# Kernel tuning notes

Hardware: AMD Instinct MI355X
Metric: run time of the kernel (lower is better)

## Reference

```python
import jax, jax.numpy as jnp
import numpy as np

B, S, H = 8, 4096, 1024
E, K = 64, 2
CAP_FACTOR = 1.25
TEMP = 1.0
LBW = 0.01


def setup_inputs() -> dict:
    key = jax.random.key(0)
    k1, k2, k3 = jax.random.split(key, 3)
    x = jax.random.normal(k1, (B, S, H), dtype=jnp.float32)
    gate_w = jax.random.normal(k2, (E, H), dtype=jnp.float32) * 0.02
    expert_w = jax.random.normal(k3, (E, H, H), dtype=jnp.float32) * 0.02
    return {"x": x, "gate_w": gate_w, "expert_w": expert_w}


def _moe_forward(x, gate_w, expert_w):
    b, s, h = x.shape
    xf = x.reshape(-1, h)                      # [N, H]
    N = xf.shape[0]
    capacity = int(N * K / E * CAP_FACTOR)

    # --- gating ---
    logits = xf @ gate_w.T                     # [N, E]
    vals, idx = jax.lax.top_k(logits / TEMP, K)  # [N, K]
    probs = jax.nn.softmax(vals, axis=-1)      # [N, K]

    # --- dispatch: first-come-first-served position within each expert ---
    ef = idx.reshape(-1)                       # [N*K], token-major order (matches torch loop)
    onehot = jax.nn.one_hot(ef, E, dtype=jnp.int32)            # [N*K, E]
    pos = jnp.take_along_axis(jnp.cumsum(onehot, axis=0), ef[:, None], axis=1)[:, 0] - 1
    valid = pos < capacity
    slot = jnp.where(valid, ef * capacity + pos, E * capacity)  # out-of-range -> dropped

    # token_map[e, c] = token_idx * K + k  (or -1 if empty)
    token_map = jnp.full((E * capacity,), -1, dtype=jnp.int32)
    token_map = token_map.at[slot].set(jnp.arange(N * K, dtype=jnp.int32), mode="drop")

    tok = jnp.clip(token_map // K, 0, N - 1)
    filled = token_map >= 0
    expert_inputs = jnp.where(filled[:, None], xf[tok], 0.0)    # [E*cap, H]
    expert_inputs = expert_inputs.reshape(E, capacity, h)

    # --- grouped expert GEMM (no bias; zero rows stay zero) ---
    expert_outputs = jnp.einsum("ech,edh->ecd", expert_inputs, expert_w)  # [E, cap, H]

    # --- combine: weighted scatter-add back to tokens ---
    eo_flat = expert_outputs.reshape(E * capacity, h)
    wk = token_map % K
    weight = jnp.where(filled, probs[tok, jnp.clip(wk, 0, K - 1)], 0.0)
    out_idx = jnp.where(filled, tok, N)        # invalid -> dropped
    output = jnp.zeros((N, h), dtype=xf.dtype).at[out_idx].add(
        weight[:, None] * eo_flat, mode="drop")

    # --- aux load-balancing loss ---
    gate_probs = jax.nn.softmax(logits, axis=-1)
    usage = jnp.bincount(ef, length=E).astype(jnp.float32) / (N * K + 1e-9)
    importance = gate_probs.mean(axis=0)
    aux = jnp.sum(usage * importance) * E
    aux = jnp.minimum(aux * LBW, 1.0)

    return output.reshape(b, s, h), aux


def reference(x, gate_w, expert_w):
    return _moe_forward(x, gate_w, expert_w)
```

## Files before the change

### kernel.cpp

```cpp
#include <hip/hip_runtime.h>
#include <hip/hip_bf16.h>

#define NTOK 32768
#define NE 64
#define HD 1024
#define CAP 1280
#define NKF (NTOK*2)
#define NSLOT (NE*CAP)
#define NTILE 256

typedef __attribute__((ext_vector_type(8))) short bf16x8;
typedef __attribute__((ext_vector_type(4))) short bf16x4;
typedef __attribute__((ext_vector_type(4))) float f32x4;
typedef __attribute__((ext_vector_type(4))) unsigned short u16x4;

__device__ __forceinline__ short f2bf(float f) {
  union { __hip_bfloat16 b; short s; } u;
  u.b = __float2bfloat16(f);
  return u.s;
}
__device__ __forceinline__ float bf2f(unsigned short h) {
  return __uint_as_float(((unsigned)h) << 16);
}

__global__ __launch_bounds__(256) void gating_kernel(const float* __restrict__ x,
                                                     const float* __restrict__ gw,
                                                     float* __restrict__ logits,
                                                     __hip_bfloat16* __restrict__ xb) {
  __shared__ float Xs[64][132];
  __shared__ float Gs[64][132];
  const int tid = threadIdx.x;
  const int tok0 = blockIdx.x * 64;
  const int th = tid >> 4;
  const int te = tid & 15;
  float acc[4][4];
#pragma unroll
  for (int i = 0; i < 4; ++i)
#pragma unroll
    for (int j = 0; j < 4; ++j) acc[i][j] = 0.f;

  for (int k0 = 0; k0 < HD; k0 += 128) {
#pragma unroll
    for (int r = 0; r < 8; ++r) {
      int idx = r * 256 + tid;
      int row = idx >> 5;
      int c = (idx & 31) * 4;
      float4 xv4 = *(const float4*)&x[(size_t)(tok0 + row) * HD + k0 + c];
      *(float4*)&Xs[row][c] = xv4;
      bf16x4 o;
      o[0] = f2bf(xv4.x); o[1] = f2bf(xv4.y); o[2] = f2bf(xv4.z); o[3] = f2bf(xv4.w);
      *(bf16x4*)&xb[(size_t)(tok0 + row) * HD + k0 + c] = o;
      *(float4*)&Gs[row][c] = *(const float4*)&gw[(size_t)row * HD + k0 + c];
    }
    __syncthreads();
#pragma unroll 4
    for (int kk = 0; kk < 32; ++kk) {
      float4 xv[4], gv[4];
#pragma unroll
      for (int i = 0; i < 4; ++i) xv[i] = *(float4*)&Xs[th + i * 16][kk * 4];
#pragma unroll
      for (int j = 0; j < 4; ++j) gv[j] = *(float4*)&Gs[te + j * 16][kk * 4];
#pragma unroll
      for (int i = 0; i < 4; ++i)
#pragma unroll
        for (int j = 0; j < 4; ++j) {
          acc[i][j] = fmaf(xv[i].x, gv[j].x, acc[i][j]);
          acc[i][j] = fmaf(xv[i].y, gv[j].y, acc[i][j]);
          acc[i][j] = fmaf(xv[i].z, gv[j].z, acc[i][j]);
          acc[i][j] = fmaf(xv[i].w, gv[j].w, acc[i][j]);
        }
    }
    __syncthreads();
  }
#pragma unroll
  for (int i = 0; i < 4; ++i)
#pragma unroll
    for (int j = 0; j < 4; ++j)
      logits[(size_t)(tok0 + th + i * 16) * NE + te + j * 16] = acc[i][j];
}

__global__ __launch_bounds__(256) void topk_kernel(const float* __restrict__ logits,
                                                   int2* __restrict__ e01,
                                                   float2* __restrict__ p01,
                                                   float* __restrict__ imp_part) {
  const int t = blockIdx.x * 256 + threadIdx.x;
  float l[64];
  const float4* lp = (const float4*)(logits + (size_t)t * NE);
#pragma unroll
  for (int i = 0; i < 16; ++i) {
    float4 v = lp[i];
    l[4 * i] = v.x; l[4 * i + 1] = v.y; l[4 * i + 2] = v.z; l[4 * i + 3] = v.w;
  }
  float v1 = -1e30f; int i1 = 0;
#pragma unroll
  for (int j = 0; j < 64; ++j) if (l[j] > v1) { v1 = l[j]; i1 = j; }
  float v2 = -1e30f; int i2 = 0;
#pragma unroll
  for (int j = 0; j < 64; ++j) if (j != i1 && l[j] > v2) { v2 = l[j]; i2 = j; }
  float ex = __expf(v2 - v1);
  float inv2 = 1.f / (1.f + ex);
  e01[t] = make_int2(i1, i2);
  p01[t] = make_float2(inv2, ex * inv2);

  float s = 0.f;
#pragma unroll
  for (int j = 0; j < 64; ++j) s += __expf(l[j] - v1);
  float invs = 1.f / s;
  const int wid = t >> 6;
#pragma unroll
  for (int e = 0; e < 64; ++e) {
    float p = __expf(l[e] - v1) * invs;
#pragma unroll
    for (int off = 32; off; off >>= 1) p += __shfl_xor(p, off);
    if ((threadIdx.x & 63) == 0) imp_part[(size_t)wid * 64 + e] = p;
  }
}

__global__ __launch_bounds__(256) void hist_rank_kernel(const int2* __restrict__ e01,
                                                        int* __restrict__ rank_buf,
                                                        int* __restrict__ hist) {
  __shared__ int wave_hist[4][64];
  const int tid = threadIdx.x;
  const int w = tid >> 6, lane = tid & 63;
  const int i = blockIdx.x * 256 + tid;
  int2 ee = e01[i >> 1];
  const int e = (i & 1) ? ee.y : ee.x;
  int rank = 0, cnt = 0;
#pragma unroll
  for (int j = 0; j < 64; ++j) {
    int ej = __shfl(e, j);
    rank += (j < lane) & (ej == e);
    cnt += (ej == lane);
  }
  wave_hist[w][lane] = cnt;
  __syncthreads();
#pragma unroll
  for (int ww = 0; ww < 4; ++ww)
    if (ww < w) rank += wave_hist[ww][e];
  rank_buf[i] = rank;
  if (tid < 64)
    hist[blockIdx.x * 64 + tid] =
        wave_hist[0][tid] + wave_hist[1][tid] + wave_hist[2][tid] + wave_hist[3][tid];
}

__global__ __launch_bounds__(64) void scan_kernel(const int* __restrict__ hist,
                                                  int* __restrict__ tile_off,
                                                  int* __restrict__ counts) {
  const int e = threadIdx.x;
  int run = 0;
  for (int t = 0; t < NTILE; ++t) {
    int h = hist[t * 64 + e];
    tile_off[t * 64 + e] = run;
    run += h;
  }
  counts[e] = run;
}

__global__ __launch_bounds__(256) void place_kernel(const int2* __restrict__ e01,
                                                    const int* __restrict__ rank_buf,
                                                    const int* __restrict__ tile_off,
                                                    int* __restrict__ slot_of,
                                                    int* __restrict__ slot_token) {
  const int tid = threadIdx.x;
  const int i = blockIdx.x * 256 + tid;
  int2 ee = e01[i >> 1];
  const int e = (i & 1) ? ee.y : ee.x;
  const int pos = tile_off[blockIdx.x * 64 + e] + rank_buf[i];
  const int slot = (pos < CAP) ? (e * CAP + pos) : -1;
  slot_of[i] = slot;
  if (slot >= 0) slot_token[slot] = i;
}

__global__ __launch_bounds__(256) void convw_kernel(const float* __restrict__ w,
                                                    __hip_bfloat16* __restrict__ wb) {
  const size_t idx = ((size_t)blockIdx.x * 256 + threadIdx.x) * 8;
  float4 a = *(const float4*)(w + idx);
  float4 b = *(const float4*)(w + idx + 4);
  bf16x8 o;
  o[0] = f2bf(a.x); o[1] = f2bf(a.y); o[2] = f2bf(a.z); o[3] = f2bf(a.w);
  o[4] = f2bf(b.x); o[5] = f2bf(b.y); o[6] = f2bf(b.z); o[7] = f2bf(b.w);
  *(bf16x8*)(wb + idx) = o;
}

#define ASYNC16(g, l) __builtin_amdgcn_global_load_lds( \
    (const __attribute__((address_space(1))) void*)(g), \
    (__attribute__((address_space(3))) void*)(l), 16, 0, 0)

#define STAGE_A(buf, ks, kcol) do {                                             \
    const int _d = ((buf) * 16384 + (ks) * 8192 + wuni) * 2;                    \
    ASYNC16(arow0 + (kcol) + (ks) * 32 + sw8, (char*)lds + _d);                 \
    ASYNC16(arow1 + (kcol) + (ks) * 32 + sw8, (char*)lds + _d + 8192);          \
  } while (0)

#define STAGE_B(buf, ks, kcol) do {                                             \
    const __hip_bfloat16* _g = B + (size_t)srow * HD + (kcol) + (ks) * 32 + sw8; \
    const int _d = (32768 + (buf) * 16384 + (ks) * 8192 + wuni) * 2;            \
    ASYNC16(_g, (char*)lds + _d);                                               \
    ASYNC16(_g + (size_t)128 * HD, (char*)lds + _d + 8192);                     \
  } while (0)

#define LDA(dst, buf, ks, mi) \
  dst = *(const bf16x8*)(lds + (buf) * 16384 + (ks) * 8192 + (wm * 128 + (mi) * 16 + fr) * 32 + rsw)
#define LDB(dst, buf, ks, ni) \
  dst = *(const bf16x8*)(lds + 32768 + (buf) * 16384 + (ks) * 8192 + (wn * 64 + (ni) * 16 + fr) * 32 + rsw)

#define MFMA_HALF(h)                                                            \
  _Pragma("unroll")                                                             \
  for (int mm = 0; mm < 4; ++mm)                                                \
    _Pragma("unroll")                                                           \
    for (int nn = 0; nn < 4; ++nn)                                              \
      acc[(h) * 4 + mm][nn] =                                                   \
          __builtin_amdgcn_mfma_f32_16x16x32_bf16(av[mm], bv[nn], acc[(h) * 4 + mm][nn], 0, 0, 0)

#define BARX() do { asm volatile("" ::: "memory"); __builtin_amdgcn_s_barrier(); asm volatile("" ::: "memory"); } while (0)

__global__ __launch_bounds__(512, 2) void moe_gemm_kernel(const __hip_bfloat16* __restrict__ xb,
                                                          const int* __restrict__ slot_token,
                                                          const __hip_bfloat16* __restrict__ Wb,
                                                          const __hip_bfloat16* __restrict__ zp,
                                                          __hip_bfloat16* __restrict__ Eo) {
  __shared__ __hip_bfloat16 lds[65536];

  const int bid = blockIdx.x;
  const int swz = (bid & 7) * 160 + (bid >> 3);
  const int e = swz / 20;
  const int t20 = swz - e * 20;
  const int tm = t20 >> 2, tn = t20 & 3;

  const int tid = threadIdx.x;
  const int lane = tid & 63;
  const int w = tid >> 6;
  const int wm = w >> 2, wn = w & 3;

  const __hip_bfloat16* B = Wb + (size_t)e * HD * HD + (size_t)(tn * 256) * HD;

  const int srow = tid >> 2;
  const int sw8 = ((tid & 3) ^ ((tid >> 3) & 3)) * 8;
  const int wuni = w * 512;

  const int slotbase = e * CAP + tm * 256;
  const int i0 = slot_token[slotbase + srow];
  const int i1 = slot_token[slotbase + 128 + srow];
  const __hip_bfloat16* arow0 = (i0 >= 0) ? xb + (size_t)(i0 >> 1) * HD : zp;
  const __hip_bfloat16* arow1 = (i1 >= 0) ? xb + (size_t)(i1 >> 1) * HD : zp;

  const int fr = lane & 15;
  const int fq = lane >> 4;
  const int rsw = (fq ^ ((fr >> 1) & 3)) * 8;

  f32x4 acc[8][4] = {};

  STAGE_A(0, 0, 0);
  STAGE_B(0, 0, 0);
  STAGE_A(0, 1, 0);
  STAGE_B(0, 1, 0);
  asm volatile("s_waitcnt vmcnt(4)" ::: "memory");
  BARX();

#pragma unroll 2
  for (int t = 0; t < 16; ++t) {
    const int cur = t & 1, nxt = cur ^ 1;
    const int kc = (t + 1) * 64;
    const bool hn = (t < 15);
    bf16x8 av[4], bv[4];

    LDB(bv[0], cur, 0, 0); LDB(bv[1], cur, 0, 1); LDB(bv[2], cur, 0, 2); LDB(bv[3], cur, 0, 3);
    LDA(av[0], cur, 0, 0); LDA(av[1], cur, 0, 1); LDA(av[2], cur, 0, 2); LDA(av[3], cur, 0, 3);
    if (hn) STAGE_A(nxt, 0, kc);
    BARX();
    __builtin_amdgcn_s_setprio(1);
    MFMA_HALF(0);
    __builtin_amdgcn_s_setprio(0);
    BARX();

    LDA(av[0], cur, 0, 4); LDA(av[1], cur, 0, 5); LDA(av[2], cur, 0, 6); LDA(av[3], cur, 0, 7);
    if (hn) {
      STAGE_B(nxt, 0, kc);
      asm volatile("s_waitcnt vmcnt(4)" ::: "memory");
    } else {
      asm volatile("s_waitcnt vmcnt(0)" ::: "memory");
    }
    BARX();
    __builtin_amdgcn_s_setprio(1);
    MFMA_HALF(1);
    __builtin_amdgcn_s_setprio(0);
    BARX();

    LDB(bv[0], cur, 1, 0); LDB(bv[1], cur, 1, 1); LDB(bv[2], cur, 1, 2); LDB(bv[3], cur, 1, 3);
    LDA(av[0], cur, 1, 0); LDA(av[1], cur, 1, 1); LDA(av[2], cur, 1, 2); LDA(av[3], cur, 1, 3);
    if (hn) STAGE_A(nxt, 1, kc);
    BARX();
    __builtin_amdgcn_s_setprio(1);
    MFMA_HALF(0);
    __builtin_amdgcn_s_setprio(0);
    BARX();

    LDA(av[0], cur, 1, 4); LDA(av[1], cur, 1, 5); LDA(av[2], cur, 1, 6); LDA(av[3], cur, 1, 7);
    if (hn) {
      STAGE_B(nxt, 1, kc);
      asm volatile("s_waitcnt vmcnt(4)" ::: "memory");
    }
    BARX();
    __builtin_amdgcn_s_setprio(1);
    MFMA_HALF(1);
    __builtin_amdgcn_s_setprio(0);
    BARX();
  }

  __hip_bfloat16* C = Eo + (size_t)e * CAP * HD +
                      (size_t)(tm * 256 + wm * 128) * HD + tn * 256 + wn * 64;
#pragma unroll
  for (int m = 0; m < 8; ++m)
#pragma unroll
    for (int n = 0; n < 4; ++n)
#pragma unroll
      for (int r = 0; r < 4; ++r)
        C[(size_t)(m * 16 + fq * 4 + r) * HD + n * 16 + fr] = __float2bfloat16(acc[m][n][r]);
}

__global__ __launch_bounds__(256) void combine_kernel(const __hip_bfloat16* __restrict__ eo,
                                                      const int* __restrict__ slot_of,
                                                      const float2* __restrict__ p01,
                                                      float* __restrict__ out) {
  const int t = blockIdx.x;
  const int tid = threadIdx.x;
  const float2 p = p01[t];
  const int s0 = slot_of[2 * t], s1 = slot_of[2 * t + 1];
  float a0 = 0.f, a1 = 0.f, a2 = 0.f, a3 = 0.f;
  if (s0 >= 0) {
    u16x4 v = *(const u16x4*)((const unsigned short*)eo + (size_t)s0 * HD + tid * 4);
    a0 += p.x * bf2f(v[0]); a1 += p.x * bf2f(v[1]);
    a2 += p.x * bf2f(v[2]); a3 += p.x * bf2f(v[3]);
  }
  if (s1 >= 0) {
    u16x4 v = *(const u16x4*)((const unsigned short*)eo + (size_t)s1 * HD + tid * 4);
    a0 += p.y * bf2f(v[0]); a1 += p.y * bf2f(v[1]);
    a2 += p.y * bf2f(v[2]); a3 += p.y * bf2f(v[3]);
  }
  float4 res = make_float4(a0, a1, a2, a3);
  *(float4*)(out + (size_t)t * HD + tid * 4) = res;
}

__global__ __launch_bounds__(64) void aux_kernel(const float* __restrict__ imp_part,
                                                 const int* __restrict__ counts,
                                                 float* __restrict__ out) {
  const int e = threadIdx.x;
  float imp = 0.f;
  for (int w = 0; w < 512; ++w) imp += imp_part[(size_t)w * 64 + e];
  imp *= (1.f / (float)NTOK);
  float usage = (float)counts[e] / (float)NKF;
  float v = usage * imp;
#pragma unroll
  for (int off = 32; off; off >>= 1) v += __shfl_xor(v, off);
  if (e == 0) out[(size_t)NTOK * HD] = fminf(v * (float)NE * 0.01f, 1.0f);
}

extern "C" void kernel_launch(void* const* d_in, const int* in_sizes, int n_in,
                              void* d_out, int out_size, void* d_ws, size_t ws_size,
                              hipStream_t stream) {
  const float* x = (const float*)d_in[0];
  const float* gw = (const float*)d_in[1];
  const float* ew = (const float*)d_in[2];
  float* out = (float*)d_out;

  char* p = (char*)d_ws;
  float* logits = (float*)p;            p += (size_t)NTOK * NE * 4;
  int2* e01 = (int2*)p;                 p += (size_t)NTOK * 8;
  float2* p01 = (float2*)p;             p += (size_t)NTOK * 8;
  int* slot_of = (int*)p;               p += (size_t)NKF * 4;
  int* slot_token = (int*)p;            p += (size_t)NSLOT * 4;
  int* counts = (int*)p;                p += 256;
  float* imp_part = (float*)p;          p += (size_t)512 * 64 * 4;
  int* rank_buf = (int*)p;              p += (size_t)NKF * 4;
  int* hist = (int*)p;                  p += (size_t)NTILE * 64 * 4;
  int* tile_off = (int*)p;              p += (size_t)NTILE * 64 * 4;
  __hip_bfloat16* zp = (__hip_bfloat16*)p; p += 4096;
  __hip_bfloat16* xb = (__hip_bfloat16*)p; p += (size_t)NTOK * HD * 2;
  __hip_bfloat16* Wb = (__hip_bfloat16*)p;  p += (size_t)NE * HD * HD * 2;
  __hip_bfloat16* Eo = (__hip_bfloat16*)p;  p += (size_t)NSLOT * HD * 2;

  hipMemsetAsync(slot_token, 0xFF, (size_t)NSLOT * 4, stream);
  hipMemsetAsync(zp, 0, 4096, stream);

  convw_kernel<<<32768, 256, 0, stream>>>(ew, Wb);
  gating_kernel<<<NTOK / 64, 256, 0, stream>>>(x, gw, logits, xb);
  topk_kernel<<<NTOK / 256, 256, 0, stream>>>(logits, e01, p01, imp_part);
  hist_rank_kernel<<<NTILE, 256, 0, stream>>>(e01, rank_buf, hist);
  scan_kernel<<<1, 64, 0, stream>>>(hist, tile_off, counts);
  place_kernel<<<NTILE, 256, 0, stream>>>(e01, rank_buf, tile_off, slot_of, slot_token);
  moe_gemm_kernel<<<dim3(1280), 512, 0, stream>>>(xb, slot_token, Wb, zp, Eo);
  combine_kernel<<<NTOK, 256, 0, stream>>>(Eo, slot_of, p01, out);
  aux_kernel<<<1, 64, 0, stream>>>(imp_part, counts, out);
}
```

Before: 442.2 us.

## Fuse weight conversion into gating kernel and merge top-k with histogram ranking

Merges the expert-weight fp32-to-bf16 conversion into the gating launch, with interleaved blocks doing either gating or a strided conversion loop, so the two memory-bound phases share one launch. It also fuses the per-token top-k with the per-tile rank and histogram computation, ranking both expert choices per token in a single wave shuffle pass. Each tile now covers 512 assignments, which halves the number of tiles the serial scan has to walk. This removes two launches and a round trip of the expert ids through global memory. The cost is a heterogeneous kernel whose block mix may load-balance unevenly.

```diff
diff --git a/kernel.cpp b/kernel.cpp
--- a/kernel.cpp
+++ b/kernel.cpp
@@ -7,7 +7,7 @@
 #define CAP 1280
 #define NKF (NTOK*2)
 #define NSLOT (NE*CAP)
-#define NTILE 256
+#define NTILE 128
 
 typedef __attribute__((ext_vector_type(8))) short bf16x8;
 typedef __attribute__((ext_vector_type(4))) short bf16x4;
@@ -23,14 +23,35 @@
   return __uint_as_float(((unsigned)h) << 16);
 }
 
-__global__ __launch_bounds__(256) void gating_kernel(const float* __restrict__ x,
-                                                     const float* __restrict__ gw,
-                                                     float* __restrict__ logits,
-                                                     __hip_bfloat16* __restrict__ xb) {
+__global__ __launch_bounds__(256) void gate_conv_kernel(const float* __restrict__ x,
+                                                        const float* __restrict__ gw,
+                                                        float* __restrict__ logits,
+                                                        __hip_bfloat16* __restrict__ xb,
+                                                        const float* __restrict__ ew,
+                                                        __hip_bfloat16* __restrict__ wb) {
   __shared__ float Xs[64][132];
   __shared__ float Gs[64][132];
+  const int bid = blockIdx.x;
   const int tid = threadIdx.x;
-  const int tok0 = blockIdx.x * 64;
+
+  if (bid >= 1024 || (bid & 1)) {
+    const int cid = (bid < 1024) ? (bid >> 1) : (bid - 512);
+    size_t i = ((size_t)cid * 256 + tid) * 8;
+    const size_t stride = (size_t)2048 * 256 * 8;
+#pragma unroll 2
+    for (int it = 0; it < 16; ++it, i += stride) {
+      float4 a = *(const float4*)(ew + i);
+      float4 b = *(const float4*)(ew + i + 4);
+      bf16x8 o;
+      o[0] = f2bf(a.x); o[1] = f2bf(a.y); o[2] = f2bf(a.z); o[3] = f2bf(a.w);
+      o[4] = f2bf(b.x); o[5] = f2bf(b.y); o[6] = f2bf(b.z); o[7] = f2bf(b.w);
+      *(bf16x8*)(wb + i) = o;
+    }
+    return;
+  }
+
+  const int gid = bid >> 1;
+  const int tok0 = gid * 64;
   const int th = tid >> 4;
   const int te = tid & 15;
   float acc[4][4];
@@ -79,11 +100,16 @@
       logits[(size_t)(tok0 + th + i * 16) * NE + te + j * 16] = acc[i][j];
 }
 
-__global__ __launch_bounds__(256) void topk_kernel(const float* __restrict__ logits,
-                                                   int2* __restrict__ e01,
-                                                   float2* __restrict__ p01,
-                                                   float* __restrict__ imp_part) {
-  const int t = blockIdx.x * 256 + threadIdx.x;
+__global__ __launch_bounds__(256) void topk_hist_kernel(const float* __restrict__ logits,
+                                                        int2* __restrict__ e01,
+                                                        float2* __restrict__ p01,
+                                                        float* __restrict__ imp_part,
+                                                        int* __restrict__ rank_buf,
+                                                        int* __restrict__ hist) {
+  __shared__ int wh[4][64];
+  const int tid = threadIdx.x;
+  const int w = tid >> 6, lane = tid & 63;
+  const int t = blockIdx.x * 256 + tid;
   float l[64];
   const float4* lp = (const float4*)(logits + (size_t)t * NE);
 #pragma unroll
@@ -112,35 +138,30 @@
     float p = __expf(l[e] - v1) * invs;
 #pragma unroll
     for (int off = 32; off; off >>= 1) p += __shfl_xor(p, off);
-    if ((threadIdx.x & 63) == 0) imp_part[(size_t)wid * 64 + e] = p;
-  }
-}
-
-__global__ __launch_bounds__(256) void hist_rank_kernel(const int2* __restrict__ e01,
-                                                        int* __restrict__ rank_buf,
-                                                        int* __restrict__ hist) {
-  __shared__ int wave_hist[4][64];
-  const int tid = threadIdx.x;
-  const int w = tid >> 6, lane = tid & 63;
-  const int i = blockIdx.x * 256 + tid;
-  int2 ee = e01[i >> 1];
-  const int e = (i & 1) ? ee.y : ee.x;
-  int rank = 0, cnt = 0;
+    if (lane == 0) imp_part[(size_t)wid * 64 + e] = p;
+  }
+
+  int r0 = 0, r1 = 0, cnt = 0;
 #pragma unroll
   for (int j = 0; j < 64; ++j) {
-    int ej = __shfl(e, j);
-    rank += (j < lane) & (ej == e);
-    cnt += (ej == lane);
-  }
-  wave_hist[w][lane] = cnt;
+    int a = __shfl(i1, j);
+    int b = __shfl(i2, j);
+    int ja = (j < lane);
+    r0 += ja & (a == i1);
+    r0 += ja & (b == i1);
+    r1 += ja & (a == i2);
+    r1 += ja & (b == i2);
+    cnt += (a == lane) + (b == lane);
+  }
+  wh[w][lane] = cnt;
   __syncthreads();
 #pragma unroll
   for (int ww = 0; ww < 4; ++ww)
-    if (ww < w) rank += wave_hist[ww][e];
-  rank_buf[i] = rank;
+    if (ww < w) { r0 += wh[ww][i1]; r1 += wh[ww][i2]; }
+  rank_buf[2 * t] = r0;
+  rank_buf[2 * t + 1] = r1;
   if (tid < 64)
-    hist[blockIdx.x * 64 + tid] =
-        wave_hist[0][tid] + wave_hist[1][tid] + wave_hist[2][tid] + wave_hist[3][tid];
+    hist[blockIdx.x * 64 + tid] = wh[0][tid] + wh[1][tid] + wh[2][tid] + wh[3][tid];
 }
 
 __global__ __launch_bounds__(64) void scan_kernel(const int* __restrict__ hist,
@@ -165,21 +186,10 @@
   const int i = blockIdx.x * 256 + tid;
   int2 ee = e01[i >> 1];
   const int e = (i & 1) ? ee.y : ee.x;
-  const int pos = tile_off[blockIdx.x * 64 + e] + rank_buf[i];
+  const int pos = tile_off[(i >> 9) * 64 + e] + rank_buf[i];
   const int slot = (pos < CAP) ? (e * CAP + pos) : -1;
   slot_of[i] = slot;
   if (slot >= 0) slot_token[slot] = i;
-}
-
-__global__ __launch_bounds__(256) void convw_kernel(const float* __restrict__ w,
-                                                    __hip_bfloat16* __restrict__ wb) {
-  const size_t idx = ((size_t)blockIdx.x * 256 + threadIdx.x) * 8;
-  float4 a = *(const float4*)(w + idx);
-  float4 b = *(const float4*)(w + idx + 4);
-  bf16x8 o;
-  o[0] = f2bf(a.x); o[1] = f2bf(a.y); o[2] = f2bf(a.z); o[3] = f2bf(a.w);
-  o[4] = f2bf(b.x); o[5] = f2bf(b.y); o[6] = f2bf(b.z); o[7] = f2bf(b.w);
-  *(bf16x8*)(wb + idx) = o;
 }
 
 #define ASYNC16(g, l) __builtin_amdgcn_global_load_lds( \
@@ -382,12 +392,10 @@
   hipMemsetAsync(slot_token, 0xFF, (size_t)NSLOT * 4, stream);
   hipMemsetAsync(zp, 0, 4096, stream);
 
-  convw_kernel<<<32768, 256, 0, stream>>>(ew, Wb);
-  gating_kernel<<<NTOK / 64, 256, 0, stream>>>(x, gw, logits, xb);
-  topk_kernel<<<NTOK / 256, 256, 0, stream>>>(logits, e01, p01, imp_part);
-  hist_rank_kernel<<<NTILE, 256, 0, stream>>>(e01, rank_buf, hist);
+  gate_conv_kernel<<<2560, 256, 0, stream>>>(x, gw, logits, xb, ew, Wb);
+  topk_hist_kernel<<<NTOK / 256, 256, 0, stream>>>(logits, e01, p01, imp_part, rank_buf, hist);
   scan_kernel<<<1, 64, 0, stream>>>(hist, tile_off, counts);
-  place_kernel<<<NTILE, 256, 0, stream>>>(e01, rank_buf, tile_off, slot_of, slot_token);
+  place_kernel<<<NKF / 256, 256, 0, stream>>>(e01, rank_buf, tile_off, slot_of, slot_token);
   moe_gemm_kernel<<<dim3(1280), 512, 0, stream>>>(xb, slot_token, Wb, zp, Eo);
   combine_kernel<<<NTOK, 256, 0, stream>>>(Eo, slot_of, p01, out);
   aux_kernel<<<1, 64, 0, stream>>>(imp_part, counts, out);
```

Result: slower. 458.9 us (+3.8%).
